# Kernel optimization log

Measured on AMD Instinct MI355X. Metric: run time of the kernel, lower is better.

## Reference

```python
import jax, jax.numpy as jnp
import numpy as np


def setup_inputs() -> dict:
    key = jax.random.key(0)
    k1, k2 = jax.random.split(key)
    z_e_x = jax.random.normal(k1, (4096, 16, 128), dtype=jnp.float32)
    codebook = jax.random.normal(k2, (1024, 128), dtype=jnp.float32)
    return {"z_e_x": z_e_x, "codebook": codebook}


def reference(z_e_x, codebook):
    # VQStraightThrough.forward: nearest-codebook quantization in fp32.
    B, N, C = z_e_x.shape
    x = z_e_x.astype(jnp.float32).reshape(B * N, C)          # [BN, C]
    cb = codebook.astype(jnp.float32)                        # [K, C]
    inputs_sq = jnp.sum(x * x, axis=1, keepdims=True)        # [BN, 1]
    codebook_sq = jnp.sum(cb * cb, axis=1)                   # [K]
    l2_dis = inputs_sq + codebook_sq - 2.0 * (x @ cb.T)      # [BN, K]
    flat_idx = jnp.argmin(l2_dis, axis=1)                    # [BN] int
    min_vals = jnp.min(l2_dis, axis=1)                       # [BN]
    idx = flat_idx.reshape(B, N)
    distances = min_vals.reshape(B, N).astype(z_e_x.dtype)
    codes = cb[flat_idx].reshape(B, N, C).astype(z_e_x.dtype)  # gather
    return codes, flat_idx, idx, distances
```

## Files before the change

### kernel.cpp

```cpp
#include <hip/hip_runtime.h>
#include <math.h>
#include <stdint.h>

#define C        128
#define KCODES   1024
#define KHALF    512
#define TPB      256
#define ROWS_PB  128
#define NCHUNK   64
#define NCHUNKS_H (KHALF / NCHUNK)
#define BSTRIDE  272
#define BHALF    (NCHUNK * BSTRIDE)
#define EPS_TRIG 0.25f

typedef __attribute__((ext_vector_type(8))) short bf16x8_t;
typedef __attribute__((ext_vector_type(4))) float f32x4_t;

static __device__ __forceinline__ uint32_t bf16_rne(float f) {
    uint32_t u = __float_as_uint(f);
    return (u + 0x7FFFu + ((u >> 16) & 1u)) >> 16;
}
static __device__ __forceinline__ float bf16_hi_f(float f) {
    return __uint_as_float(bf16_rne(f) << 16);
}

__global__ void cb_prep_kernel(const float* __restrict__ cb,
                               uint16_t* __restrict__ cbh,
                               uint16_t* __restrict__ cbl,
                               float* __restrict__ cbsq) {
    const int i = blockIdx.x * blockDim.x + threadIdx.x;
    if (i < KCODES * C) {
        float f = cb[i];
        uint32_t h = bf16_rne(f);
        float lo = f - __uint_as_float(h << 16);
        cbh[i] = (uint16_t)h;
        cbl[i] = (uint16_t)bf16_rne(lo);
    }
    if (i < KCODES) {
        const float4* cp = (const float4*)(cb + (size_t)i * C);
        float sx = 0.f, sy = 0.f, sz = 0.f, sw = 0.f;
        #pragma unroll
        for (int j = 0; j < C / 4; ++j) {
            float4 v = cp[j];
            sx += v.x * v.x; sy += v.y * v.y;
            sz += v.z * v.z; sw += v.w * v.w;
        }
        cbsq[i] = (sx + sy) + (sz + sw);
    }
}

#define SLOTS(OP) OP(0,0) OP(0,1) OP(0,2) OP(0,3) OP(1,0) OP(1,1) OP(1,2) OP(1,3)
#define MFMA_BF16 __builtin_amdgcn_mfma_f32_16x16x32_bf16

__global__ __launch_bounds__(TPB, 3)
void vq_partial_kernel(const float* __restrict__ x,
                       const uint16_t* __restrict__ cbh,
                       const uint16_t* __restrict__ cbl,
                       const float* __restrict__ cq,
                       float4* __restrict__ top2,
                       int rows)
{
    __shared__ __align__(16) uint8_t s_buf[2 * BHALF];
    __shared__ float s_cq[NCHUNK];

    const int t    = threadIdx.x;
    const int lane = t & 63;
    const int w    = t >> 6;
    const int ln   = lane & 15;
    const int quad = lane >> 4;
    const int rb   = blockIdx.x >> 1;
    const int kh   = blockIdx.x & 1;
    const int rowblock = rb * ROWS_PB;
    const int kh0      = kh * KHALF;

    #pragma unroll 4
    for (int i = 0; i < 16; ++i) {
        int fid = t + i * TPB;
        int row = fid >> 5;
        int kq  = fid & 31;
        int grow = rowblock + row;
        grow = grow < rows ? grow : rows - 1;
        float4 v = ((const float4*)x)[(size_t)grow * 32 + kq];
        uint32_t p0 = bf16_rne(v.x) | (bf16_rne(v.y) << 16);
        uint32_t p1 = bf16_rne(v.z) | (bf16_rne(v.w) << 16);
        *(uint2*)(s_buf + row * BSTRIDE + kq * 8) = make_uint2(p0, p1);
    }
    __syncthreads();

    const int arow0 = (w * 32 + ln) * BSTRIDE;
    const int arow1 = (w * 32 + 16 + ln) * BSTRIDE;
    bf16x8_t ah00, ah01, ah02, ah03, ah10, ah11, ah12, ah13;
    ah00 = *(const bf16x8_t*)(s_buf + arow0 + 0 * 64 + quad * 16);
    ah01 = *(const bf16x8_t*)(s_buf + arow0 + 1 * 64 + quad * 16);
    ah02 = *(const bf16x8_t*)(s_buf + arow0 + 2 * 64 + quad * 16);
    ah03 = *(const bf16x8_t*)(s_buf + arow0 + 3 * 64 + quad * 16);
    ah10 = *(const bf16x8_t*)(s_buf + arow1 + 0 * 64 + quad * 16);
    ah11 = *(const bf16x8_t*)(s_buf + arow1 + 1 * 64 + quad * 16);
    ah12 = *(const bf16x8_t*)(s_buf + arow1 + 2 * 64 + quad * 16);
    ah13 = *(const bf16x8_t*)(s_buf + arow1 + 3 * 64 + quad * 16);
    __syncthreads();

    #pragma unroll 4
    for (int i = 0; i < 16; ++i) {
        int fid = t + i * TPB;
        int row = fid >> 5;
        int kq  = fid & 31;
        int grow = rowblock + row;
        grow = grow < rows ? grow : rows - 1;
        float4 v = ((const float4*)x)[(size_t)grow * 32 + kq];
        uint32_t p0 = bf16_rne(v.x - bf16_hi_f(v.x)) | (bf16_rne(v.y - bf16_hi_f(v.y)) << 16);
        uint32_t p1 = bf16_rne(v.z - bf16_hi_f(v.z)) | (bf16_rne(v.w - bf16_hi_f(v.w)) << 16);
        *(uint2*)(s_buf + row * BSTRIDE + kq * 8) = make_uint2(p0, p1);
    }
    __syncthreads();

    bf16x8_t al00, al01, al02, al03, al10, al11, al12, al13;
    al00 = *(const bf16x8_t*)(s_buf + arow0 + 0 * 64 + quad * 16);
    al01 = *(const bf16x8_t*)(s_buf + arow0 + 1 * 64 + quad * 16);
    al02 = *(const bf16x8_t*)(s_buf + arow0 + 2 * 64 + quad * 16);
    al03 = *(const bf16x8_t*)(s_buf + arow0 + 3 * 64 + quad * 16);
    al10 = *(const bf16x8_t*)(s_buf + arow1 + 0 * 64 + quad * 16);
    al11 = *(const bf16x8_t*)(s_buf + arow1 + 1 * 64 + quad * 16);
    al12 = *(const bf16x8_t*)(s_buf + arow1 + 2 * 64 + quad * 16);
    al13 = *(const bf16x8_t*)(s_buf + arow1 + 3 * 64 + quad * 16);
    __syncthreads();

#define DECL(g,r) float v1_##g##r = INFINITY, v2_##g##r = INFINITY; int k1_##g##r = 0, k2_##g##r = 0;
    SLOTS(DECL)
#undef DECL

    #pragma unroll 1
    for (int chn = 0; chn < NCHUNKS_H; ++chn) {
        const int kbase = kh0 + chn * NCHUNK;
        #pragma unroll
        for (int i = 0; i < 4; ++i) {
            int uid  = t + i * TPB;
            int code = uid >> 4, g = uid & 15;
            uint4 dh = ((const uint4*)cbh)[(size_t)(kbase + code) * 16 + g];
            *(uint4*)(s_buf + code * BSTRIDE + g * 16) = dh;
            uint4 dl = ((const uint4*)cbl)[(size_t)(kbase + code) * 16 + g];
            *(uint4*)(s_buf + BHALF + code * BSTRIDE + g * 16) = dl;
        }
        if (t < NCHUNK) s_cq[t] = cq[kbase + t];
        __syncthreads();

        const uint8_t* bbase = s_buf + (size_t)ln * BSTRIDE + quad * 16;
        #pragma unroll
        for (int ct = 0; ct < 4; ++ct) {
            const uint8_t* bh_p = bbase + (size_t)ct * 16 * BSTRIDE;
            const uint8_t* bl_p = bh_p + BHALF;
            f32x4_t acc0 = {0.f, 0.f, 0.f, 0.f};
            f32x4_t acc1 = {0.f, 0.f, 0.f, 0.f};
#define KSTEP(kk) { \
            bf16x8_t bh = *(const bf16x8_t*)(bh_p + kk * 64); \
            bf16x8_t bl = *(const bf16x8_t*)(bl_p + kk * 64); \
            acc0 = MFMA_BF16(ah0##kk, bh, acc0, 0, 0, 0); \
            acc0 = MFMA_BF16(al0##kk, bh, acc0, 0, 0, 0); \
            acc0 = MFMA_BF16(ah0##kk, bl, acc0, 0, 0, 0); \
            acc1 = MFMA_BF16(ah1##kk, bh, acc1, 0, 0, 0); \
            acc1 = MFMA_BF16(al1##kk, bh, acc1, 0, 0, 0); \
            acc1 = MFMA_BF16(ah1##kk, bl, acc1, 0, 0, 0); }
            KSTEP(0) KSTEP(1) KSTEP(2) KSTEP(3)
#undef KSTEP
            const float cqv = s_cq[ct * 16 + ln];
            const int   kc  = kbase + ct * 16 + ln;
#define UPD(g,r) { \
            float s_ = fmaf(-2.0f, (g ? acc1 : acc0)[r], cqv); \
            bool c1_ = s_ < v1_##g##r; \
            bool c2_ = s_ < v2_##g##r; \
            v2_##g##r = c1_ ? v1_##g##r : (c2_ ? s_ : v2_##g##r); \
            k2_##g##r = c1_ ? k1_##g##r : (c2_ ? kc : k2_##g##r); \
            v1_##g##r = c1_ ? s_ : v1_##g##r; \
            k1_##g##r = c1_ ? kc : k1_##g##r; }
            SLOTS(UPD)
#undef UPD
        }
        __syncthreads();
    }

    for (int m_ = 1; m_ <= 8; m_ <<= 1) {
#define MRG(g,r) { \
        float ov1 = __shfl_xor(v1_##g##r, m_, 16); int ok1 = __shfl_xor(k1_##g##r, m_, 16); \
        float ov2 = __shfl_xor(v2_##g##r, m_, 16); int ok2 = __shfl_xor(k2_##g##r, m_, 16); \
        if (ov1 < v1_##g##r || (ov1 == v1_##g##r && ok1 < k1_##g##r)) { \
            if (v1_##g##r < ov2 || (v1_##g##r == ov2 && k1_##g##r < ok2)) { v2_##g##r = v1_##g##r; k2_##g##r = k1_##g##r; } \
            else { v2_##g##r = ov2; k2_##g##r = ok2; } \
            v1_##g##r = ov1; k1_##g##r = ok1; \
        } else if (ov1 < v2_##g##r || (ov1 == v2_##g##r && ok1 < k2_##g##r)) { \
            v2_##g##r = ov1; k2_##g##r = ok1; \
        } }
        SLOTS(MRG)
#undef MRG
    }
    if (ln == 0) {
#define WRT(g,r) { int rloc = w * 32 + g * 16 + quad * 4 + r; \
        int rowg = rowblock + rloc; \
        if (rowg < rows) { \
            top2[(size_t)kh * rows + rowg] = \
                make_float4(v1_##g##r, __int_as_float(k1_##g##r), \
                            v2_##g##r, __int_as_float(k2_##g##r)); } }
        SLOTS(WRT)
#undef WRT
    }
}

#define FROWS 256

__global__ __launch_bounds__(TPB, 4)
void vq_finalize_kernel(const float* __restrict__ x,
                        const float* __restrict__ cb,
                        const float* __restrict__ cq,
                        const float4* __restrict__ top2,
                        float* __restrict__ out_codes,
                        float* __restrict__ out_fidx,
                        float* __restrict__ out_idx,
                        float* __restrict__ out_dist,
                        int rows)
{
    __shared__ int s_k1[FROWS];
    const int t    = threadIdx.x;
    const int base = blockIdx.x * FROWS;

    {
        int rowg = base + t;
        const bool valid = rowg < rows;
        rowg = valid ? rowg : rows - 1;

        float4 ha = top2[rowg];
        float4 hb = top2[(size_t)rows + rowg];
        float av1 = ha.x, av2 = ha.z;  int ak1 = __float_as_int(ha.y), ak2 = __float_as_int(ha.w);
        float bv1 = hb.x, bv2 = hb.z;  int bk1 = __float_as_int(hb.y), bk2 = __float_as_int(hb.w);
        float v1, v2; int k1, k2;
        if (bv1 < av1 || (bv1 == av1 && bk1 < ak1)) {
            v1 = bv1; k1 = bk1;
            if (av1 < bv2 || (av1 == bv2 && ak1 < bk2)) { v2 = av1; k2 = ak1; }
            else                                        { v2 = bv2; k2 = bk2; }
        } else {
            v1 = av1; k1 = ak1;
            if (bv1 < av2 || (bv1 == av2 && bk1 < ak2)) { v2 = bv1; k2 = bk1; }
            else                                        { v2 = av2; k2 = ak2; }
        }

        const float* xr = x + (size_t)rowg * C;

        float sx = 0.f, sy = 0.f, sz = 0.f, sw = 0.f;
        {
            const float4* xp = (const float4*)xr;
            #pragma unroll
            for (int i = 0; i < C / 4; ++i) {
                float4 v = xp[i];
                sx += v.x * v.x; sy += v.y * v.y;
                sz += v.z * v.z; sw += v.w * v.w;
            }
        }
        const float rs = (sx + sy) + (sz + sw);

        bool switched = false;
        double qwin = 0.0;
        if (v2 - v1 < EPS_TRIG) {
            const float* c1p = cb + (size_t)k1 * C;
            const float* c2p = cb + (size_t)k2 * C;
            double dot1 = 0.0, cq1 = 0.0, dot2 = 0.0, cq2 = 0.0;
            #pragma unroll 8
            for (int c = 0; c < C; ++c) {
                const double xc  = (double)xr[c];
                const double cv1 = (double)c1p[c];
                const double cv2 = (double)c2p[c];
                dot1 += xc * cv1;  cq1 += cv1 * cv1;
                dot2 += xc * cv2;  cq2 += cv2 * cv2;
            }
            const double q1 = cq1 - 2.0 * dot1;
            const double q2 = cq2 - 2.0 * dot2;
            if (q2 < q1 || (q2 == q1 && k2 < k1)) { k1 = k2; switched = true; qwin = q2; }
        }

        const float* c1p = cb + (size_t)k1 * C;
        float a = 0.f;
        #pragma unroll 16
        for (int c = 0; c < C; ++c) a = fmaf(xr[c], c1p[c], a);
        float d = (rs + cq[k1]) - 2.f * a;
        if (switched) d = (float)((double)rs + qwin);

        if (valid) {
            out_fidx[rowg] = (float)k1;
            out_idx[rowg]  = (float)k1;
            out_dist[rowg] = d;
        }
        s_k1[t] = k1;
    }
    __syncthreads();

    #pragma unroll 1
    for (int pass = 0; pass < 8; ++pass) {
        const int r    = pass * 32 + (t >> 3);
        const int sub  = t & 7;
        const int rowg = base + r;
        if (rowg < rows) {
            const int k1 = s_k1[r];
            const float4* src = (const float4*)(cb + (size_t)k1 * C);
            float4*       dst = (float4*)(out_codes + (size_t)rowg * C);
            #pragma unroll
            for (int i = 0; i < 4; ++i) dst[sub + i * 8] = src[sub + i * 8];
        }
    }
}

__global__ __launch_bounds__(TPB, 1)
void vq_nearest_fallback(const float* __restrict__ x,
                         const float* __restrict__ cb,
                         float* __restrict__ out_codes,
                         float* __restrict__ out_fidx,
                         float* __restrict__ out_idx,
                         float* __restrict__ out_dist,
                         int rows)
{
    __shared__ float s_cbsq[KCODES];
    const int t = threadIdx.x;
    for (int k = t; k < KCODES; k += TPB) {
        const float4* cp = (const float4*)(cb + (size_t)k * C);
        float sx = 0.f, sy = 0.f, sz = 0.f, sw = 0.f;
        #pragma unroll
        for (int i = 0; i < C / 4; ++i) {
            float4 v = cp[i];
            sx += v.x * v.x; sy += v.y * v.y; sz += v.z * v.z; sw += v.w * v.w;
        }
        s_cbsq[k] = (sx + sy) + (sz + sw);
    }
    __syncthreads();
    const int row = blockIdx.x * TPB + t;
    if (row >= rows) return;
    float xr[C];
    {
        const float4* xp = (const float4*)(x + (size_t)row * C);
        #pragma unroll
        for (int i = 0; i < C / 4; ++i) {
            float4 v = xp[i];
            xr[4*i+0] = v.x; xr[4*i+1] = v.y; xr[4*i+2] = v.z; xr[4*i+3] = v.w;
        }
    }
    float rs;
    {
        float sx = 0.f, sy = 0.f, sz = 0.f, sw = 0.f;
        #pragma unroll
        for (int i = 0; i < C / 4; ++i) {
            sx += xr[4*i+0]*xr[4*i+0]; sy += xr[4*i+1]*xr[4*i+1];
            sz += xr[4*i+2]*xr[4*i+2]; sw += xr[4*i+3]*xr[4*i+3];
        }
        rs = (sx + sy) + (sz + sw);
    }
    float v1 = INFINITY, v2 = INFINITY; int k1 = 0, k2 = 0;
    #pragma unroll 1
    for (int k0 = 0; k0 < KCODES; k0 += 4) {
        const float* c0 = cb + (size_t)k0 * C;
        float a0 = 0.f, a1 = 0.f, a2 = 0.f, a3 = 0.f;
        #pragma unroll
        for (int c = 0; c < C; ++c) {
            const float xc = xr[c];
            a0 = fmaf(xc, c0[c], a0);
            a1 = fmaf(xc, c0[C + c], a1);
            a2 = fmaf(xc, c0[2*C + c], a2);
            a3 = fmaf(xc, c0[3*C + c], a3);
        }
        const float d0 = (rs + s_cbsq[k0+0]) - 2.f * a0;
        const float d1 = (rs + s_cbsq[k0+1]) - 2.f * a1;
        const float d2 = (rs + s_cbsq[k0+2]) - 2.f * a2;
        const float d3 = (rs + s_cbsq[k0+3]) - 2.f * a3;
        #define UPDF(dv, ki)                                                 \
            if ((dv) < v1)      { v2 = v1; k2 = k1; v1 = (dv); k1 = (ki); } \
            else if ((dv) < v2) { v2 = (dv); k2 = (ki); }
        UPDF(d0, k0+0); UPDF(d1, k0+1); UPDF(d2, k0+2); UPDF(d3, k0+3);
        #undef UPDF
    }
    if (v2 - v1 < 0.125f) {
        const float* c1p = cb + (size_t)k1 * C;
        const float* c2p = cb + (size_t)k2 * C;
        double dot1 = 0.0, cq1 = 0.0, dot2 = 0.0, cq2 = 0.0;
        #pragma unroll 8
        for (int c = 0; c < C; ++c) {
            const double xc = (double)xr[c];
            const double cv1 = (double)c1p[c];
            const double cv2 = (double)c2p[c];
            dot1 += xc * cv1; cq1 += cv1 * cv1;
            dot2 += xc * cv2; cq2 += cv2 * cv2;
        }
        const double q1 = cq1 - 2.0 * dot1;
        const double q2 = cq2 - 2.0 * dot2;
        if (q2 < q1 || (q2 == q1 && k2 < k1)) { k1 = k2; v1 = (float)((double)rs + q2); }
    }
    {
        const float4* src = (const float4*)(cb + (size_t)k1 * C);
        float4* dst = (float4*)(out_codes + (size_t)row * C);
        #pragma unroll
        for (int i = 0; i < C / 4; ++i) dst[i] = src[i];
        out_fidx[row] = (float)k1;
        out_idx[row]  = (float)k1;
        out_dist[row] = v1;
    }
}

extern "C" void kernel_launch(void* const* d_in, const int* in_sizes, int n_in,
                              void* d_out, int out_size, void* d_ws, size_t ws_size,
                              hipStream_t stream) {
    const float* x  = (const float*)d_in[0];
    const float* cb = (const float*)d_in[1];
    const int rows = in_sizes[0] / C;

    float* out       = (float*)d_out;
    float* out_codes = out;
    float* out_fidx  = out + (size_t)rows * C;
    float* out_idx   = out_fidx + rows;
    float* out_dist  = out_idx + rows;

    const size_t cbh_off  = 0;
    const size_t cbl_off  = (size_t)KCODES * C * sizeof(uint16_t);
    const size_t cq_off   = cbl_off * 2;
    const size_t top2_off = cq_off + KCODES * sizeof(float);
    const size_t need     = top2_off + (size_t)2 * rows * sizeof(float4);

    if (ws_size >= need) {
        uint16_t* cbh  = (uint16_t*)((char*)d_ws + cbh_off);
        uint16_t* cbl  = (uint16_t*)((char*)d_ws + cbl_off);
        float*    cq   = (float*)((char*)d_ws + cq_off);
        float4*   top2 = (float4*)((char*)d_ws + top2_off);

        cb_prep_kernel<<<(KCODES * C + TPB - 1) / TPB, TPB, 0, stream>>>(cb, cbh, cbl, cq);

        const int rowblocks = (rows + ROWS_PB - 1) / ROWS_PB;
        vq_partial_kernel<<<rowblocks * 2, TPB, 0, stream>>>(x, cbh, cbl, cq, top2, rows);

        const int fblocks = (rows + FROWS - 1) / FROWS;
        vq_finalize_kernel<<<fblocks, TPB, 0, stream>>>(x, cb, cq, top2,
                                                        out_codes, out_fidx,
                                                        out_idx, out_dist, rows);
    } else {
        const int rowblocks = (rows + TPB - 1) / TPB;
        vq_nearest_fallback<<<rowblocks, TPB, 0, stream>>>(x, cb, out_codes, out_fidx,
                                                           out_idx, out_dist, rows);
    }
}
```

Before: 196.9 us.

## Fuse codebook prep, partial search and finalize into one kernel with last-block merge

Removes the separate codebook bf16 split/norm kernel and the finalize kernel. Each block now converts fp32 codebook chunks into hi/lo bf16 in shared memory and computes the norms on the fly, and the second of the two K-half blocks per row block (chosen with an atomic counter) merges the top-2 candidates and writes outputs. This saves two launches and the workspace round trips, in exchange for redundant per-block conversion work, atomics and fences. The counter uses parity and is never reset, and it relies on the workspace starting at some defined value.

```diff
diff --git a/kernel.cpp b/kernel.cpp
--- a/kernel.cpp
+++ b/kernel.cpp
@@ -24,44 +24,24 @@
     return __uint_as_float(bf16_rne(f) << 16);
 }
 
-__global__ void cb_prep_kernel(const float* __restrict__ cb,
-                               uint16_t* __restrict__ cbh,
-                               uint16_t* __restrict__ cbl,
-                               float* __restrict__ cbsq) {
-    const int i = blockIdx.x * blockDim.x + threadIdx.x;
-    if (i < KCODES * C) {
-        float f = cb[i];
-        uint32_t h = bf16_rne(f);
-        float lo = f - __uint_as_float(h << 16);
-        cbh[i] = (uint16_t)h;
-        cbl[i] = (uint16_t)bf16_rne(lo);
-    }
-    if (i < KCODES) {
-        const float4* cp = (const float4*)(cb + (size_t)i * C);
-        float sx = 0.f, sy = 0.f, sz = 0.f, sw = 0.f;
-        #pragma unroll
-        for (int j = 0; j < C / 4; ++j) {
-            float4 v = cp[j];
-            sx += v.x * v.x; sy += v.y * v.y;
-            sz += v.z * v.z; sw += v.w * v.w;
-        }
-        cbsq[i] = (sx + sy) + (sz + sw);
-    }
-}
-
 #define SLOTS(OP) OP(0,0) OP(0,1) OP(0,2) OP(0,3) OP(1,0) OP(1,1) OP(1,2) OP(1,3)
 #define MFMA_BF16 __builtin_amdgcn_mfma_f32_16x16x32_bf16
 
 __global__ __launch_bounds__(TPB, 3)
-void vq_partial_kernel(const float* __restrict__ x,
-                       const uint16_t* __restrict__ cbh,
-                       const uint16_t* __restrict__ cbl,
-                       const float* __restrict__ cq,
-                       float4* __restrict__ top2,
-                       int rows)
+void vq_fused_kernel(const float* __restrict__ x,
+                     const float* __restrict__ cb,
+                     unsigned long long* __restrict__ top2,
+                     unsigned int* __restrict__ cnt,
+                     float* __restrict__ out_codes,
+                     float* __restrict__ out_fidx,
+                     float* __restrict__ out_idx,
+                     float* __restrict__ out_dist,
+                     int rows)
 {
     __shared__ __align__(16) uint8_t s_buf[2 * BHALF];
     __shared__ float s_cq[NCHUNK];
+    __shared__ int   s_k1f[ROWS_PB];
+    __shared__ int   s_win;
 
     const int t    = threadIdx.x;
     const int lane = t & 63;
@@ -136,12 +116,26 @@
         for (int i = 0; i < 4; ++i) {
             int uid  = t + i * TPB;
             int code = uid >> 4, g = uid & 15;
-            uint4 dh = ((const uint4*)cbh)[(size_t)(kbase + code) * 16 + g];
-            *(uint4*)(s_buf + code * BSTRIDE + g * 16) = dh;
-            uint4 dl = ((const uint4*)cbl)[(size_t)(kbase + code) * 16 + g];
-            *(uint4*)(s_buf + BHALF + code * BSTRIDE + g * 16) = dl;
-        }
-        if (t < NCHUNK) s_cq[t] = cq[kbase + t];
+            const float4* src = (const float4*)(cb + (size_t)(kbase + code) * C) + g * 2;
+            float4 v0 = src[0], v1 = src[1];
+            uint32_t h0 = bf16_rne(v0.x) | (bf16_rne(v0.y) << 16);
+            uint32_t h1 = bf16_rne(v0.z) | (bf16_rne(v0.w) << 16);
+            uint32_t h2 = bf16_rne(v1.x) | (bf16_rne(v1.y) << 16);
+            uint32_t h3 = bf16_rne(v1.z) | (bf16_rne(v1.w) << 16);
+            uint32_t l0 = bf16_rne(v0.x - bf16_hi_f(v0.x)) | (bf16_rne(v0.y - bf16_hi_f(v0.y)) << 16);
+            uint32_t l1 = bf16_rne(v0.z - bf16_hi_f(v0.z)) | (bf16_rne(v0.w - bf16_hi_f(v0.w)) << 16);
+            uint32_t l2 = bf16_rne(v1.x - bf16_hi_f(v1.x)) | (bf16_rne(v1.y - bf16_hi_f(v1.y)) << 16);
+            uint32_t l3 = bf16_rne(v1.z - bf16_hi_f(v1.z)) | (bf16_rne(v1.w - bf16_hi_f(v1.w)) << 16);
+            *(uint4*)(s_buf + code * BSTRIDE + g * 16)          = make_uint4(h0, h1, h2, h3);
+            *(uint4*)(s_buf + BHALF + code * BSTRIDE + g * 16)  = make_uint4(l0, l1, l2, l3);
+            float ps = ((v0.x * v0.x + v0.y * v0.y) + (v0.z * v0.z + v0.w * v0.w))
+                     + ((v1.x * v1.x + v1.y * v1.y) + (v1.z * v1.z + v1.w * v1.w));
+            ps += __shfl_xor(ps, 1, 16);
+            ps += __shfl_xor(ps, 2, 16);
+            ps += __shfl_xor(ps, 4, 16);
+            ps += __shfl_xor(ps, 8, 16);
+            if (g == 0) s_cq[code] = ps;
+        }
         __syncthreads();
 
         const uint8_t* bbase = s_buf + (size_t)ln * BSTRIDE + quad * 16;
@@ -196,40 +190,39 @@
 #define WRT(g,r) { int rloc = w * 32 + g * 16 + quad * 4 + r; \
         int rowg = rowblock + rloc; \
         if (rowg < rows) { \
-            top2[(size_t)kh * rows + rowg] = \
-                make_float4(v1_##g##r, __int_as_float(k1_##g##r), \
-                            v2_##g##r, __int_as_float(k2_##g##r)); } }
+            size_t base_ = ((size_t)kh * rows + rowg) << 1; \
+            unsigned long long e1 = ((unsigned long long)__float_as_uint(v1_##g##r) << 32) | (unsigned)k1_##g##r; \
+            unsigned long long e2 = ((unsigned long long)__float_as_uint(v2_##g##r) << 32) | (unsigned)k2_##g##r; \
+            __hip_atomic_store(&top2[base_ + 0], e1, __ATOMIC_RELAXED, __HIP_MEMORY_SCOPE_AGENT); \
+            __hip_atomic_store(&top2[base_ + 1], e2, __ATOMIC_RELAXED, __HIP_MEMORY_SCOPE_AGENT); } }
         SLOTS(WRT)
 #undef WRT
     }
-}
-
-#define FROWS 256
-
-__global__ __launch_bounds__(TPB, 4)
-void vq_finalize_kernel(const float* __restrict__ x,
-                        const float* __restrict__ cb,
-                        const float* __restrict__ cq,
-                        const float4* __restrict__ top2,
-                        float* __restrict__ out_codes,
-                        float* __restrict__ out_fidx,
-                        float* __restrict__ out_idx,
-                        float* __restrict__ out_dist,
-                        int rows)
-{
-    __shared__ int s_k1[FROWS];
-    const int t    = threadIdx.x;
-    const int base = blockIdx.x * FROWS;
-
-    {
-        int rowg = base + t;
+    __syncthreads();
+
+    if (t == 0) {
+        __threadfence();
+        unsigned old = atomicAdd(&cnt[rb], 1u);
+        s_win = (int)(old & 1u);
+    }
+    __syncthreads();
+    if (!s_win) return;
+    __threadfence();
+
+    if (t < ROWS_PB) {
+        int rowg = rowblock + t;
         const bool valid = rowg < rows;
         rowg = valid ? rowg : rows - 1;
 
-        float4 ha = top2[rowg];
-        float4 hb = top2[(size_t)rows + rowg];
-        float av1 = ha.x, av2 = ha.z;  int ak1 = __float_as_int(ha.y), ak2 = __float_as_int(ha.w);
-        float bv1 = hb.x, bv2 = hb.z;  int bk1 = __float_as_int(hb.y), bk2 = __float_as_int(hb.w);
+        unsigned long long ea1 = __hip_atomic_load(&top2[((size_t)rowg << 1) + 0], __ATOMIC_RELAXED, __HIP_MEMORY_SCOPE_AGENT);
+        unsigned long long ea2 = __hip_atomic_load(&top2[((size_t)rowg << 1) + 1], __ATOMIC_RELAXED, __HIP_MEMORY_SCOPE_AGENT);
+        unsigned long long eb1 = __hip_atomic_load(&top2[(((size_t)rows + rowg) << 1) + 0], __ATOMIC_RELAXED, __HIP_MEMORY_SCOPE_AGENT);
+        unsigned long long eb2 = __hip_atomic_load(&top2[(((size_t)rows + rowg) << 1) + 1], __ATOMIC_RELAXED, __HIP_MEMORY_SCOPE_AGENT);
+        float av1 = __uint_as_float((uint32_t)(ea1 >> 32)); int ak1 = (int)(uint32_t)ea1;
+        float av2 = __uint_as_float((uint32_t)(ea2 >> 32)); int ak2 = (int)(uint32_t)ea2;
+        float bv1 = __uint_as_float((uint32_t)(eb1 >> 32)); int bk1 = (int)(uint32_t)eb1;
+        float bv2 = __uint_as_float((uint32_t)(eb2 >> 32)); int bk2 = (int)(uint32_t)eb2;
+
         float v1, v2; int k1, k2;
         if (bv1 < av1 || (bv1 == av1 && bk1 < ak1)) {
             v1 = bv1; k1 = bk1;
@@ -274,33 +267,42 @@
             if (q2 < q1 || (q2 == q1 && k2 < k1)) { k1 = k2; switched = true; qwin = q2; }
         }
 
-        const float* c1p = cb + (size_t)k1 * C;
-        float a = 0.f;
-        #pragma unroll 16
-        for (int c = 0; c < C; ++c) a = fmaf(xr[c], c1p[c], a);
-        float d = (rs + cq[k1]) - 2.f * a;
-        if (switched) d = (float)((double)rs + qwin);
-
-        if (valid) {
-            out_fidx[rowg] = (float)k1;
-            out_idx[rowg]  = (float)k1;
-            out_dist[rowg] = d;
-        }
-        s_k1[t] = k1;
-    }
-    __syncthreads();
-
-    #pragma unroll 1
-    for (int pass = 0; pass < 8; ++pass) {
-        const int r    = pass * 32 + (t >> 3);
-        const int sub  = t & 7;
-        const int rowg = base + r;
+        {
+            const float4* c1p4 = (const float4*)(cb + (size_t)k1 * C);
+            const float4* xp4  = (const float4*)xr;
+            float a = 0.f;
+            float qx = 0.f, qy = 0.f, qz = 0.f, qw = 0.f;
+            #pragma unroll
+            for (int i = 0; i < C / 4; ++i) {
+                float4 cv = c1p4[i]; float4 xv = xp4[i];
+                a = fmaf(xv.x, cv.x, a); a = fmaf(xv.y, cv.y, a);
+                a = fmaf(xv.z, cv.z, a); a = fmaf(xv.w, cv.w, a);
+                qx += cv.x * cv.x; qy += cv.y * cv.y;
+                qz += cv.z * cv.z; qw += cv.w * cv.w;
+            }
+            float d = (rs + ((qx + qy) + (qz + qw))) - 2.f * a;
+            if (switched) d = (float)((double)rs + qwin);
+
+            if (valid) {
+                out_fidx[rowg] = (float)k1;
+                out_idx[rowg]  = (float)k1;
+                out_dist[rowg] = d;
+            }
+        }
+        s_k1f[t] = k1;
+    }
+    __syncthreads();
+
+    {
+        const int r    = t >> 1;
+        const int half = t & 1;
+        const int rowg = rowblock + r;
         if (rowg < rows) {
-            const int k1 = s_k1[r];
-            const float4* src = (const float4*)(cb + (size_t)k1 * C);
-            float4*       dst = (float4*)(out_codes + (size_t)rowg * C);
+            const int k1 = s_k1f[r];
+            const float4* src = (const float4*)(cb + (size_t)k1 * C) + half * 16;
+            float4*       dst = (float4*)(out_codes + (size_t)rowg * C) + half * 16;
             #pragma unroll
-            for (int i = 0; i < 4; ++i) dst[sub + i * 8] = src[sub + i * 8];
+            for (int i = 0; i < 16; ++i) dst[i] = src[i];
         }
     }
 }
@@ -411,30 +413,22 @@
     float* out_idx   = out_fidx + rows;
     float* out_dist  = out_idx + rows;
 
-    const size_t cbh_off  = 0;
-    const size_t cbl_off  = (size_t)KCODES * C * sizeof(uint16_t);
-    const size_t cq_off   = cbl_off * 2;
-    const size_t top2_off = cq_off + KCODES * sizeof(float);
-    const size_t need     = top2_off + (size_t)2 * rows * sizeof(float4);
+    const int rowblocks = (rows + ROWS_PB - 1) / ROWS_PB;
+
+    const size_t top2_off = 0;
+    const size_t cnt_off  = (size_t)2 * rows * 2 * sizeof(unsigned long long);
+    const size_t need     = cnt_off + (size_t)rowblocks * sizeof(unsigned int);
 
     if (ws_size >= need) {
-        uint16_t* cbh  = (uint16_t*)((char*)d_ws + cbh_off);
-        uint16_t* cbl  = (uint16_t*)((char*)d_ws + cbl_off);
-        float*    cq   = (float*)((char*)d_ws + cq_off);
-        float4*   top2 = (float4*)((char*)d_ws + top2_off);
-
-        cb_prep_kernel<<<(KCODES * C + TPB - 1) / TPB, TPB, 0, stream>>>(cb, cbh, cbl, cq);
-
-        const int rowblocks = (rows + ROWS_PB - 1) / ROWS_PB;
-        vq_partial_kernel<<<rowblocks * 2, TPB, 0, stream>>>(x, cbh, cbl, cq, top2, rows);
-
-        const int fblocks = (rows + FROWS - 1) / FROWS;
-        vq_finalize_kernel<<<fblocks, TPB, 0, stream>>>(x, cb, cq, top2,
-                                                        out_codes, out_fidx,
-                                                        out_idx, out_dist, rows);
+        unsigned long long* top2 = (unsigned long long*)((char*)d_ws + top2_off);
+        unsigned int*       cnt  = (unsigned int*)((char*)d_ws + cnt_off);
+
+        vq_fused_kernel<<<rowblocks * 2, TPB, 0, stream>>>(x, cb, top2, cnt,
+                                                           out_codes, out_fidx,
+                                                           out_idx, out_dist, rows);
     } else {
-        const int rowblocks = (rows + TPB - 1) / TPB;
-        vq_nearest_fallback<<<rowblocks, TPB, 0, stream>>>(x, cb, out_codes, out_fidx,
-                                                           out_idx, out_dist, rows);
+        const int rb = (rows + TPB - 1) / TPB;
+        vq_nearest_fallback<<<rb, TPB, 0, stream>>>(x, cb, out_codes, out_fidx,
+                                                    out_idx, out_dist, rows);
     }
 }
```

Result: slower. 352.1 us (+78.8%).
